# Performance work log

Measured on AMD Instinct MI355X. Metric: run time of the kernel, lower is better.

## Reference

```python
import jax, jax.numpy as jnp
import numpy as np

H = 2048
EPS = 1e-5

def _layernorm(x, g, b):
    mu = jnp.mean(x, axis=-1, keepdims=True)
    var = jnp.mean(jnp.square(x - mu), axis=-1, keepdims=True)
    return (x - mu) * jax.lax.rsqrt(var + EPS) * g + b

def setup_inputs() -> dict:
    key = jax.random.key(0)
    ks = jax.random.split(key, 12)
    s = 1.0 / np.sqrt(H)
    inp = {
        "x": jax.random.normal(ks[0], (2, 2048, H), dtype=jnp.float32),
        "ln1_g": jnp.ones((H,), jnp.float32),
        "ln1_b": jnp.zeros((H,), jnp.float32),
        "ln2_g": jnp.ones((H,), jnp.float32),
        "ln2_b": jnp.zeros((H,), jnp.float32),
        "qkv_w": jax.random.uniform(ks[1], (H, 3 * H), jnp.float32, -s, s),
        "qkv_b": jax.random.uniform(ks[2], (3 * H,), jnp.float32, -s, s),
        "out_w": jax.random.uniform(ks[3], (H, H), jnp.float32, -s, s),
        "out_b": jax.random.uniform(ks[4], (H,), jnp.float32, -s, s),
        "mlp_w1": jax.random.uniform(ks[5], (H, 4 * H), jnp.float32, -s, s),
        "mlp_b1": jax.random.uniform(ks[6], (4 * H,), jnp.float32, -s, s),
        "mlp_w2": jax.random.uniform(ks[7], (4 * H, H), jnp.float32, -1.0 / np.sqrt(4 * H), 1.0 / np.sqrt(4 * H)),
        "mlp_b2": jax.random.uniform(ks[8], (H,), jnp.float32, -1.0 / np.sqrt(4 * H), 1.0 / np.sqrt(4 * H)),
    }
    return inp

def reference(x, ln1_g, ln1_b, ln2_g, ln2_b, qkv_w, qkv_b, out_w, out_b, mlp_w1, mlp_b1, mlp_w2, mlp_b2):
    residual = x
    h = _layernorm(x, ln1_g, ln1_b)
    qkv = h @ qkv_w + qkv_b                      # [B,S,3H]
    q, k, v = jnp.split(qkv, 3, axis=-1)         # each [B,S,H] (single-head attention)
    scores = jnp.einsum('bsh,bth->bst', q, k) / jnp.sqrt(jnp.float32(H))
    attn = jax.nn.softmax(scores, axis=-1)
    attn_out = jnp.einsum('bst,bth->bsh', attn, v)
    attn_out = attn_out @ out_w + out_b
    x = residual + attn_out                      # dropout is identity in eval
    residual = x
    h = _layernorm(x, ln2_g, ln2_b)
    h = jax.nn.gelu(h @ mlp_w1 + mlp_b1, approximate=False)
    h = h @ mlp_w2 + mlp_b2
    return residual + h
```

## Files before the change

kernel.cpp:

```cpp
#include <hip/hip_runtime.h>
#include <hip/hip_bf16.h>
#include <math.h>

typedef __bf16 bf16_t;
typedef __bf16 bf16x8 __attribute__((ext_vector_type(8)));
typedef __bf16 bf16x4 __attribute__((ext_vector_type(4)));
typedef float  f32x4  __attribute__((ext_vector_type(4)));

enum { EPI_BF16_BIAS = 0, EPI_F32_SCALE = 1, EPI_BF16 = 2, EPI_F32_BIAS_RES = 3, EPI_BF16_BIAS_GELU = 4 };

__device__ __forceinline__ float gelu_exact(float v) {
  return 0.5f * v * (1.0f + erff(v * 0.7071067811865476f));
}

__device__ __forceinline__ void gld_lds16(const bf16_t* g, bf16_t* l) {
  __builtin_amdgcn_global_load_lds(
      (const __attribute__((address_space(1))) uint32_t*)(uintptr_t)g,
      (__attribute__((address_space(3))) uint32_t*)(uintptr_t)l, 16, 0, 0);
}

#define SB()    __builtin_amdgcn_s_barrier()
#define LGKM0() do { asm volatile("s_waitcnt lgkmcnt(0)" ::: "memory"); __builtin_amdgcn_sched_barrier(0); } while(0)
#define VMW(N)  asm volatile("s_waitcnt vmcnt(" #N ")" ::: "memory")
#define LGKMW(N) asm volatile("s_waitcnt lgkmcnt(" #N ")" ::: "memory")

#define RD(base, rowbase, ks) \
  (*(const bf16x8*)((base) + ((rowbase) + lr) * 64 + (((((ks) << 2) | lg)) ^ (lr & 7)) * 8))

#define DO_MFMA(IBASE, JBASE) \
  __builtin_amdgcn_s_setprio(1); \
  { _Pragma("unroll") for (int ii = 0; ii < 4; ++ii) \
    _Pragma("unroll") for (int jj = 0; jj < 2; ++jj) \
    _Pragma("unroll") for (int ks = 0; ks < 2; ++ks) \
      acc[(IBASE)+ii][(JBASE)+jj] = __builtin_amdgcn_mfma_f32_16x16x32_bf16( \
          aF[ii][ks], bF[jj][ks], acc[(IBASE)+ii][(JBASE)+jj], 0, 0, 0); } \
  __builtin_amdgcn_s_setprio(0);

template<int EPI>
__global__ __launch_bounds__(512, 2) void tb_gemm8(
    const bf16_t* __restrict__ A, int lda, long long strideA,
    const bf16_t* __restrict__ B, int ldb, long long strideB,
    const float* __restrict__ bias,
    const float* __restrict__ resid,
    void* __restrict__ Cp, int ldc, long long strideC,
    int K, float scale)
{
  __shared__ __align__(16) bf16_t sm[65536];

  const int tid = threadIdx.x;
  const int lane = tid & 63;
  const int wid = tid >> 6;
  const int wm = wid >> 2;
  const int wn = wid & 3;
  const int lr = lane & 15;
  const int lg = lane >> 4;
  const int z = blockIdx.z;
  const int m0 = blockIdx.y * 256;
  const int n0 = blockIdx.x * 256;

  const bf16_t* Ag = A + (size_t)z * strideA + (size_t)m0 * lda;
  const bf16_t* Bg = B + (size_t)z * strideB + (size_t)n0 * ldb;

  const int l3 = lane >> 3;
  const int sl8 = ((lane & 7) ^ l3) << 3;

  f32x4 acc[8][4];
#pragma unroll
  for (int i = 0; i < 8; ++i)
#pragma unroll
    for (int j = 0; j < 4; ++j) acc[i][j] = (f32x4){0.f, 0.f, 0.f, 0.f};

  auto stageM = [&](const bf16_t* G, int ld, bf16_t* dst, int kt, int H) {
#pragma unroll
    for (int q = 0; q < 2; ++q) {
      int c = (wid << 1) + q;
      int row = (H << 7) + (c << 3) + l3;
      gld_lds16(G + (size_t)row * ld + kt + sl8, dst + (H << 13) + (c << 9) + lane * 8);
    }
  };

  const int NT = K >> 6;
  stageM(Ag, lda, sm, 0, 0);
  stageM(Bg, ldb, sm + 16384, 0, 0);
  stageM(Bg, ldb, sm + 16384, 0, 1);
  stageM(Ag, lda, sm, 0, 1);
  VMW(4);
  SB();

  bf16x8 aF[4][2], bF[2][2];

  for (int t = 0; t < NT; ++t) {
    bf16_t* cura = sm + ((t & 1) << 15);
    bf16_t* curb = cura + 16384;
    bf16_t* nxta = sm + (((t + 1) & 1) << 15);
    bf16_t* nxtb = nxta + 16384;
    const int ktn = (t + 1) << 6;
    const bool last = (t == NT - 1);

#pragma unroll
    for (int ii = 0; ii < 4; ++ii) {
      aF[ii][0] = RD(cura, ii * 32 + wm * 16, 0);
      aF[ii][1] = RD(cura, ii * 32 + wm * 16, 1);
    }
#pragma unroll
    for (int jj = 0; jj < 2; ++jj) {
      bF[jj][0] = RD(curb, jj * 64 + wn * 16, 0);
      bF[jj][1] = RD(curb, jj * 64 + wn * 16, 1);
    }
    if (!last) stageM(Ag, lda, nxta, ktn, 0);
    if (last) { VMW(2); } else { VMW(4); }
    LGKMW(8);
    SB();
    LGKM0();
    DO_MFMA(0, 0);
    SB();

#pragma unroll
    for (int jj = 0; jj < 2; ++jj) {
      bF[jj][0] = RD(curb, 128 + jj * 64 + wn * 16, 0);
      bF[jj][1] = RD(curb, 128 + jj * 64 + wn * 16, 1);
    }
    if (!last) stageM(Bg, ldb, nxtb, ktn, 0);
    if (last) { VMW(0); } else { VMW(4); }
    SB();
    LGKM0();
    DO_MFMA(0, 2);
    SB();

#pragma unroll
    for (int ii = 0; ii < 4; ++ii) {
      aF[ii][0] = RD(cura, 128 + ii * 32 + wm * 16, 0);
      aF[ii][1] = RD(cura, 128 + ii * 32 + wm * 16, 1);
    }
    if (!last) stageM(Bg, ldb, nxtb, ktn, 1);
    SB();
    LGKM0();
    DO_MFMA(4, 2);
    SB();

#pragma unroll
    for (int jj = 0; jj < 2; ++jj) {
      bF[jj][0] = RD(curb, jj * 64 + wn * 16, 0);
      bF[jj][1] = RD(curb, jj * 64 + wn * 16, 1);
    }
    if (!last) {
      stageM(Ag, lda, nxta, ktn, 1);
      VMW(4);
    }
    SB();
    LGKM0();
    DO_MFMA(4, 0);
    SB();
  }

#pragma unroll
  for (int i = 0; i < 8; ++i) {
    const int mr = ((i >> 2) << 7) + ((i & 3) << 5) + (wm << 4);
#pragma unroll
    for (int j = 0; j < 4; ++j) {
      const int nc = ((j >> 1) << 7) + ((j & 1) << 6) + (wn << 4);
#pragma unroll
      for (int r = 0; r < 4; ++r) {
        int row = m0 + mr + lg * 4 + r;
        int col = n0 + nc + lr;
        float v = acc[i][j][r] * scale;
        if constexpr (EPI == EPI_BF16_BIAS || EPI == EPI_F32_BIAS_RES || EPI == EPI_BF16_BIAS_GELU)
          v += bias[col];
        if constexpr (EPI == EPI_BF16_BIAS_GELU)
          v = gelu_exact(v);
        if constexpr (EPI == EPI_F32_BIAS_RES)
          v += resid[(size_t)row * ldc + col];
        if constexpr (EPI == EPI_BF16_BIAS || EPI == EPI_BF16 || EPI == EPI_BF16_BIAS_GELU) {
          ((bf16_t*)Cp)[(size_t)z * strideC + (size_t)row * ldc + col] = (bf16_t)v;
        } else {
          ((float*)Cp)[(size_t)z * strideC + (size_t)row * ldc + col] = v;
        }
      }
    }
  }
}

__global__ __launch_bounds__(256) void tb_combine(
    const float* __restrict__ x2, const float* __restrict__ p0,
    const float* __restrict__ p1, const float* __restrict__ bias,
    float* __restrict__ out)
{
  size_t o = ((size_t)blockIdx.x * 256 + threadIdx.x) * 4;
  float4 a = *(const float4*)(x2 + o);
  float4 b = *(const float4*)(p0 + o);
  float4 c = *(const float4*)(p1 + o);
  float4 bb = *(const float4*)(bias + (o & 2047));
  float4 r;
  r.x = a.x + b.x + c.x + bb.x;
  r.y = a.y + b.y + c.y + bb.y;
  r.z = a.z + b.z + c.z + bb.z;
  r.w = a.w + b.w + c.w + bb.w;
  *(float4*)(out + o) = r;
}

__global__ __launch_bounds__(256) void tb_transpose_cast(
    const float* __restrict__ in, bf16_t* __restrict__ outT, int R, int C)
{
  __shared__ float tile[32][33];
  int c0 = blockIdx.x * 32;
  int r0 = blockIdx.y * 32;
  int t = threadIdx.x;
  int r = t >> 3;
  int c4 = (t & 7) * 4;
  float4 d = *(const float4*)(in + (size_t)(r0 + r) * C + c0 + c4);
  tile[r][c4 + 0] = d.x; tile[r][c4 + 1] = d.y; tile[r][c4 + 2] = d.z; tile[r][c4 + 3] = d.w;
  __syncthreads();
  int c = t >> 3;
  int r4 = (t & 7) * 4;
  bf16x4 o;
  o[0] = (bf16_t)tile[r4 + 0][c];
  o[1] = (bf16_t)tile[r4 + 1][c];
  o[2] = (bf16_t)tile[r4 + 2][c];
  o[3] = (bf16_t)tile[r4 + 3][c];
  *(bf16x4*)(outT + (size_t)(c0 + c) * R + r0 + r4) = o;
}

__global__ __launch_bounds__(256) void tb_transpose_bf16(
    const bf16_t* __restrict__ in, int ldin, long long sIn,
    bf16_t* __restrict__ out, int ldout, long long sOut)
{
  __shared__ bf16_t tile[32][40];
  int z = blockIdx.z;
  const bf16_t* src = in + (size_t)z * sIn;
  bf16_t* dst = out + (size_t)z * sOut;
  int c0 = blockIdx.x * 32;
  int r0 = blockIdx.y * 32;
  int t = threadIdx.x;
  int r = t >> 3;
  int c4 = (t & 7) * 4;
  bf16x4 d = *(const bf16x4*)(src + (size_t)(r0 + r) * ldin + c0 + c4);
  *(bf16x4*)&tile[r][c4] = d;
  __syncthreads();
  int c = t >> 3;
  int r4 = (t & 7) * 4;
  bf16x4 o;
  o[0] = tile[r4 + 0][c];
  o[1] = tile[r4 + 1][c];
  o[2] = tile[r4 + 2][c];
  o[3] = tile[r4 + 3][c];
  *(bf16x4*)(dst + (size_t)(c0 + c) * ldout + r0 + r4) = o;
}

__global__ __launch_bounds__(256) void tb_layernorm(
    const float* __restrict__ x, const float* __restrict__ g, const float* __restrict__ b,
    bf16_t* __restrict__ h)
{
  __shared__ float sa[4], sb[4];
  int row = blockIdx.x;
  int t = threadIdx.x;
  const float* xr = x + (size_t)row * 2048;
  float4 v0 = *(const float4*)(xr + t * 8);
  float4 v1 = *(const float4*)(xr + t * 8 + 4);
  float a[8] = {v0.x, v0.y, v0.z, v0.w, v1.x, v1.y, v1.z, v1.w};
  float s = 0.f, q = 0.f;
#pragma unroll
  for (int j = 0; j < 8; ++j) { s += a[j]; q += a[j] * a[j]; }
#pragma unroll
  for (int o = 32; o; o >>= 1) { s += __shfl_down(s, o); q += __shfl_down(q, o); }
  int w = t >> 6, l = t & 63;
  if (l == 0) { sa[w] = s; sb[w] = q; }
  __syncthreads();
  if (t == 0) {
    sa[0] = sa[0] + sa[1] + sa[2] + sa[3];
    sb[0] = sb[0] + sb[1] + sb[2] + sb[3];
  }
  __syncthreads();
  float mu = sa[0] * (1.0f / 2048.0f);
  float var = sb[0] * (1.0f / 2048.0f) - mu * mu;
  float rs = rsqrtf(var + 1e-5f);
  float4 g0 = *(const float4*)(g + t * 8);
  float4 g1 = *(const float4*)(g + t * 8 + 4);
  float4 b0 = *(const float4*)(b + t * 8);
  float4 b1 = *(const float4*)(b + t * 8 + 4);
  float gv[8] = {g0.x, g0.y, g0.z, g0.w, g1.x, g1.y, g1.z, g1.w};
  float bv[8] = {b0.x, b0.y, b0.z, b0.w, b1.x, b1.y, b1.z, b1.w};
  bf16x8 o8;
#pragma unroll
  for (int j = 0; j < 8; ++j) o8[j] = (bf16_t)((a[j] - mu) * rs * gv[j] + bv[j]);
  *(bf16x8*)(h + (size_t)row * 2048 + t * 8) = o8;
}

__global__ __launch_bounds__(256) void tb_softmax(
    const float* __restrict__ S, bf16_t* __restrict__ P)
{
  __shared__ float sa[4];
  int row = blockIdx.x;
  int t = threadIdx.x;
  const float* sr = S + (size_t)row * 2048;
  float4 a0 = *(const float4*)(sr + t * 8);
  float4 a1 = *(const float4*)(sr + t * 8 + 4);
  float v[8] = {a0.x, a0.y, a0.z, a0.w, a1.x, a1.y, a1.z, a1.w};
  float m = v[0];
#pragma unroll
  for (int j = 1; j < 8; ++j) m = fmaxf(m, v[j]);
#pragma unroll
  for (int o = 32; o; o >>= 1) m = fmaxf(m, __shfl_down(m, o));
  int w = t >> 6, l = t & 63;
  if (l == 0) sa[w] = m;
  __syncthreads();
  if (t == 0) sa[0] = fmaxf(fmaxf(sa[0], sa[1]), fmaxf(sa[2], sa[3]));
  __syncthreads();
  m = sa[0];
  __syncthreads();
  float s = 0.f;
#pragma unroll
  for (int j = 0; j < 8; ++j) { v[j] = expf(v[j] - m); s += v[j]; }
#pragma unroll
  for (int o = 32; o; o >>= 1) s += __shfl_down(s, o);
  if (l == 0) sa[w] = s;
  __syncthreads();
  if (t == 0) sa[0] = sa[0] + sa[1] + sa[2] + sa[3];
  __syncthreads();
  float inv = 1.0f / sa[0];
  bf16x8 o8;
#pragma unroll
  for (int j = 0; j < 8; ++j) o8[j] = (bf16_t)(v[j] * inv);
  *(bf16x8*)(P + (size_t)row * 2048 + t * 8) = o8;
}

extern "C" void kernel_launch(void* const* d_in, const int* in_sizes, int n_in,
                              void* d_out, int out_size, void* d_ws, size_t ws_size,
                              hipStream_t stream) {
  const float* x     = (const float*)d_in[0];
  const float* ln1_g = (const float*)d_in[1];
  const float* ln1_b = (const float*)d_in[2];
  const float* ln2_g = (const float*)d_in[3];
  const float* ln2_b = (const float*)d_in[4];
  const float* qkv_w = (const float*)d_in[5];
  const float* qkv_b = (const float*)d_in[6];
  const float* out_w = (const float*)d_in[7];
  const float* out_b = (const float*)d_in[8];
  const float* w1    = (const float*)d_in[9];
  const float* b1    = (const float*)d_in[10];
  const float* w2    = (const float*)d_in[11];
  const float* b2    = (const float*)d_in[12];
  float* out = (float*)d_out;
  char* ws = (char*)d_ws;

  bf16_t* qkv_wT = (bf16_t*)(ws + 0);
  bf16_t* out_wT = (bf16_t*)(ws + 25165824);
  bf16_t* w1T    = (bf16_t*)(ws + 33554432);
  bf16_t* w2T    = (bf16_t*)(ws + 67108864);
  bf16_t* h_bf   = (bf16_t*)(ws + 100663296);
  bf16_t* qkv_bf = (bf16_t*)(ws + 117440512);
  float*  scores = (float*)(ws + 167772160);
  bf16_t* attn_bf= (bf16_t*)(ws + 201326592);
  bf16_t* ao_bf  = (bf16_t*)(ws + 218103808);
  float*  x2     = (float*)(ws + 234881024);
  bf16_t* mid_bf = (bf16_t*)(ws + 117440512);
  bf16_t* Vt     = (bf16_t*)(ws + 234881024);
  float*  part0  = (float*)(ws + 0);
  float*  part1  = (float*)(ws + 201326592);

  const float inv_sqrt_h = 0.022097086912079608f;

  tb_transpose_cast<<<dim3(6144 / 32, 2048 / 32), 256, 0, stream>>>(qkv_w, qkv_wT, 2048, 6144);
  tb_transpose_cast<<<dim3(2048 / 32, 2048 / 32), 256, 0, stream>>>(out_w, out_wT, 2048, 2048);
  tb_transpose_cast<<<dim3(8192 / 32, 2048 / 32), 256, 0, stream>>>(w1, w1T, 2048, 8192);
  tb_transpose_cast<<<dim3(2048 / 32, 8192 / 32), 256, 0, stream>>>(w2, w2T, 8192, 2048);

  tb_layernorm<<<4096, 256, 0, stream>>>(x, ln1_g, ln1_b, h_bf);

  tb_gemm8<EPI_BF16_BIAS><<<dim3(24, 16, 1), 512, 0, stream>>>(
      h_bf, 2048, 0, qkv_wT, 2048, 0, qkv_b, nullptr, qkv_bf, 6144, 0, 2048, 1.0f);

  tb_transpose_bf16<<<dim3(64, 64, 2), 256, 0, stream>>>(
      qkv_bf + 4096, 6144, 2048LL * 6144, Vt, 2048, 2048LL * 2048);

  tb_gemm8<EPI_F32_SCALE><<<dim3(8, 8, 2), 512, 0, stream>>>(
      qkv_bf, 6144, 2048LL * 6144, qkv_bf + 2048, 6144, 2048LL * 6144,
      nullptr, nullptr, scores, 2048, 2048LL * 2048, 2048, inv_sqrt_h);

  tb_softmax<<<4096, 256, 0, stream>>>(scores, attn_bf);

  tb_gemm8<EPI_BF16><<<dim3(8, 8, 2), 512, 0, stream>>>(
      attn_bf, 2048, 2048LL * 2048, Vt, 2048, 2048LL * 2048,
      nullptr, nullptr, ao_bf, 2048, 2048LL * 2048, 2048, 1.0f);

  tb_gemm8<EPI_F32_BIAS_RES><<<dim3(8, 16, 1), 512, 0, stream>>>(
      ao_bf, 2048, 0, out_wT, 2048, 0, out_b, x, x2, 2048, 0, 2048, 1.0f);

  tb_layernorm<<<4096, 256, 0, stream>>>(x2, ln2_g, ln2_b, h_bf);

  tb_gemm8<EPI_BF16_BIAS_GELU><<<dim3(32, 16, 1), 512, 0, stream>>>(
      h_bf, 2048, 0, w1T, 2048, 0, b1, nullptr, mid_bf, 8192, 0, 2048, 1.0f);

  tb_gemm8<EPI_F32_SCALE><<<dim3(8, 16, 2), 512, 0, stream>>>(
      mid_bf, 8192, 4096, w2T, 8192, 4096,
      nullptr, nullptr, part0, 2048, 50331648LL, 4096, 1.0f);

  tb_combine<<<8192, 256, 0, stream>>>(x2, part0, part1, b2, out);
}
```

Measured before the change: 745.7 us.

## Replace four-phase ping-pong GEMM schedule with simple double-buffered loop

Replaces the hand-tuned four-quadrant schedule with a plain double-buffered loop. Each iteration issues all global-to-LDS loads for the next tile up front, reads all B fragments once and A fragments in two halves, runs two large MFMA blocks, then waits on vmcnt(0) and a single barrier. This removes most intra-iteration barriers and fine-grained waitcnt choreography and reuses B fragments across both A halves. In exchange it holds more fragment registers, and the full vmcnt(0) wait at iteration end can expose load latency that the staggered schedule used to hide.

```diff
diff --git a/kernel.cpp b/kernel.cpp
--- a/kernel.cpp
+++ b/kernel.cpp
@@ -20,21 +20,11 @@
 }
 
 #define SB()    __builtin_amdgcn_s_barrier()
-#define LGKM0() do { asm volatile("s_waitcnt lgkmcnt(0)" ::: "memory"); __builtin_amdgcn_sched_barrier(0); } while(0)
-#define VMW(N)  asm volatile("s_waitcnt vmcnt(" #N ")" ::: "memory")
-#define LGKMW(N) asm volatile("s_waitcnt lgkmcnt(" #N ")" ::: "memory")
+#define SCHED() __builtin_amdgcn_sched_barrier(0)
+#define VMW0()  asm volatile("s_waitcnt vmcnt(0)" ::: "memory")
 
 #define RD(base, rowbase, ks) \
   (*(const bf16x8*)((base) + ((rowbase) + lr) * 64 + (((((ks) << 2) | lg)) ^ (lr & 7)) * 8))
-
-#define DO_MFMA(IBASE, JBASE) \
-  __builtin_amdgcn_s_setprio(1); \
-  { _Pragma("unroll") for (int ii = 0; ii < 4; ++ii) \
-    _Pragma("unroll") for (int jj = 0; jj < 2; ++jj) \
-    _Pragma("unroll") for (int ks = 0; ks < 2; ++ks) \
-      acc[(IBASE)+ii][(JBASE)+jj] = __builtin_amdgcn_mfma_f32_16x16x32_bf16( \
-          aF[ii][ks], bF[jj][ks], acc[(IBASE)+ii][(JBASE)+jj], 0, 0, 0); } \
-  __builtin_amdgcn_s_setprio(0);
 
 template<int EPI>
 __global__ __launch_bounds__(512, 2) void tb_gemm8(
@@ -70,87 +60,71 @@
 #pragma unroll
     for (int j = 0; j < 4; ++j) acc[i][j] = (f32x4){0.f, 0.f, 0.f, 0.f};
 
-  auto stageM = [&](const bf16_t* G, int ld, bf16_t* dst, int kt, int H) {
-#pragma unroll
-    for (int q = 0; q < 2; ++q) {
-      int c = (wid << 1) + q;
-      int row = (H << 7) + (c << 3) + l3;
-      gld_lds16(G + (size_t)row * ld + kt + sl8, dst + (H << 13) + (c << 9) + lane * 8);
-    }
+  auto stage = [&](int par, int kt) {
+    bf16_t* da = sm + (par << 15);
+    bf16_t* db = da + 16384;
+#pragma unroll
+    for (int h = 0; h < 2; ++h)
+#pragma unroll
+      for (int q = 0; q < 2; ++q) {
+        int c = (wid << 1) + q;
+        int row = (h << 7) + (c << 3) + l3;
+        gld_lds16(Ag + (size_t)row * lda + kt + sl8, da + (h << 13) + (c << 9) + lane * 8);
+        gld_lds16(Bg + (size_t)row * ldb + kt + sl8, db + (h << 13) + (c << 9) + lane * 8);
+      }
   };
 
   const int NT = K >> 6;
-  stageM(Ag, lda, sm, 0, 0);
-  stageM(Bg, ldb, sm + 16384, 0, 0);
-  stageM(Bg, ldb, sm + 16384, 0, 1);
-  stageM(Ag, lda, sm, 0, 1);
-  VMW(4);
+  stage(0, 0);
+  VMW0();
   SB();
 
-  bf16x8 aF[4][2], bF[2][2];
-
   for (int t = 0; t < NT; ++t) {
-    bf16_t* cura = sm + ((t & 1) << 15);
-    bf16_t* curb = cura + 16384;
-    bf16_t* nxta = sm + (((t + 1) & 1) << 15);
-    bf16_t* nxtb = nxta + 16384;
-    const int ktn = (t + 1) << 6;
-    const bool last = (t == NT - 1);
-
+    SCHED();
+    const bf16_t* cura = sm + ((t & 1) << 15);
+    const bf16_t* curb = cura + 16384;
+    if (t + 1 < NT) stage((t + 1) & 1, (t + 1) << 6);
+
+    bf16x8 bF[4][2], aF[4][2];
+#pragma unroll
+    for (int jj = 0; jj < 4; ++jj) {
+      bF[jj][0] = RD(curb, jj * 64 + wn * 16, 0);
+      bF[jj][1] = RD(curb, jj * 64 + wn * 16, 1);
+    }
 #pragma unroll
     for (int ii = 0; ii < 4; ++ii) {
       aF[ii][0] = RD(cura, ii * 32 + wm * 16, 0);
       aF[ii][1] = RD(cura, ii * 32 + wm * 16, 1);
     }
-#pragma unroll
-    for (int jj = 0; jj < 2; ++jj) {
-      bF[jj][0] = RD(curb, jj * 64 + wn * 16, 0);
-      bF[jj][1] = RD(curb, jj * 64 + wn * 16, 1);
-    }
-    if (!last) stageM(Ag, lda, nxta, ktn, 0);
-    if (last) { VMW(2); } else { VMW(4); }
-    LGKMW(8);
-    SB();
-    LGKM0();
-    DO_MFMA(0, 0);
-    SB();
-
-#pragma unroll
-    for (int jj = 0; jj < 2; ++jj) {
-      bF[jj][0] = RD(curb, 128 + jj * 64 + wn * 16, 0);
-      bF[jj][1] = RD(curb, 128 + jj * 64 + wn * 16, 1);
-    }
-    if (!last) stageM(Bg, ldb, nxtb, ktn, 0);
-    if (last) { VMW(0); } else { VMW(4); }
-    SB();
-    LGKM0();
-    DO_MFMA(0, 2);
-    SB();
-
+    __builtin_amdgcn_s_setprio(1);
+#pragma unroll
+    for (int ii = 0; ii < 4; ++ii)
+#pragma unroll
+      for (int jj = 0; jj < 4; ++jj)
+#pragma unroll
+        for (int ks = 0; ks < 2; ++ks)
+          acc[ii][jj] = __builtin_amdgcn_mfma_f32_16x16x32_bf16(aF[ii][ks], bF[jj][ks], acc[ii][jj], 0, 0, 0);
+    __builtin_amdgcn_s_setprio(0);
 #pragma unroll
     for (int ii = 0; ii < 4; ++ii) {
       aF[ii][0] = RD(cura, 128 + ii * 32 + wm * 16, 0);
       aF[ii][1] = RD(cura, 128 + ii * 32 + wm * 16, 1);
     }
-    if (!last) stageM(Bg, ldb, nxtb, ktn, 1);
-    SB();
-    LGKM0();
-    DO_MFMA(4, 2);
-    SB();
-
-#pragma unroll
-    for (int jj = 0; jj < 2; ++jj) {
-      bF[jj][0] = RD(curb, jj * 64 + wn * 16, 0);
-      bF[jj][1] = RD(curb, jj * 64 + wn * 16, 1);
-    }
-    if (!last) {
-      stageM(Ag, lda, nxta, ktn, 1);
-      VMW(4);
-    }
-    SB();
-    LGKM0();
-    DO_MFMA(4, 0);
-    SB();
+    __builtin_amdgcn_s_setprio(1);
+#pragma unroll
+    for (int ii = 0; ii < 4; ++ii)
+#pragma unroll
+      for (int jj = 0; jj < 4; ++jj)
+#pragma unroll
+        for (int ks = 0; ks < 2; ++ks)
+          acc[4 + ii][jj] = __builtin_amdgcn_mfma_f32_16x16x32_bf16(aF[ii][ks], bF[jj][ks], acc[4 + ii][jj], 0, 0, 0);
+    __builtin_amdgcn_s_setprio(0);
+
+    SCHED();
+    if (t + 1 < NT) {
+      VMW0();
+      SB();
+    }
   }
 
 #pragma unroll
@@ -158,7 +132,7 @@
     const int mr = ((i >> 2) << 7) + ((i & 3) << 5) + (wm << 4);
 #pragma unroll
     for (int j = 0; j < 4; ++j) {
-      const int nc = ((j >> 1) << 7) + ((j & 1) << 6) + (wn << 4);
+      const int nc = j * 64 + (wn << 4);
 #pragma unroll
       for (int r = 0; r < 4; ++r) {
         int row = m0 + mr + lg * 4 + r;
```

After: 734.5 us. Within noise of the previous version (-1.5%).
